# Kernel optimization log

Measured on AMD Instinct MI355X. Metric: run time of the kernel, lower is better.

The kernel has to match this reference:

```python
import jax, jax.numpy as jnp
import numpy as np

VOCAB, EMB, HID = 32000, 512, 512
B, S = 4, 2048


def _log_g(x):
    # log of g(x) where g(x) = x + 0.5 for x >= 0 else sigmoid(x)
    return jnp.where(x >= 0, jnp.log(jax.nn.relu(x) + 0.5), -jax.nn.softplus(-x))


def _layernorm(x, gamma, beta, eps):
    mu = jnp.mean(x, axis=-1, keepdims=True)
    var = jnp.mean(jnp.square(x - mu), axis=-1, keepdims=True)
    return (x - mu) * jax.lax.rsqrt(var + eps) * gamma + beta


def _mingru_layer(x, W):
    # x: [B,S,D_in], W: [D_in, 2*H] (no bias for minGRU)
    k, h_pre = jnp.split(x @ W, 2, axis=-1)          # gate pre-act, candidate pre-act
    log_coeffs = -jax.nn.softplus(k)                 # log(1 - z)
    log_b = -jax.nn.softplus(-k) + _log_g(h_pre)     # log(z) + log(g(h~))
    # Heinsen log-domain parallel scan along time axis
    a_star = jnp.cumsum(log_coeffs, axis=1)          # [B,S,H]
    log_h = a_star + jax.lax.cumlogsumexp(log_b - a_star, axis=1)
    return jnp.exp(log_h)


def setup_inputs() -> dict:
    key = jax.random.key(0)
    ks = jax.random.split(key, 8)
    s = 0.02
    return {
        "ids": jax.random.randint(ks[0], (B, S), 0, VOCAB, dtype=jnp.int32),
        "emb": jax.random.normal(ks[1], (VOCAB, EMB), jnp.float32) * s,
        "W0": jax.random.normal(ks[2], (EMB, 2 * HID), jnp.float32) * s,
        "W1": jax.random.normal(ks[3], (HID, 2 * HID), jnp.float32) * s,
        "ln0_g": jnp.ones((EMB,), jnp.float32),
        "ln0_b": jnp.zeros((EMB,), jnp.float32),
        "ln1_g": jnp.ones((HID,), jnp.float32),
        "ln1_b": jnp.zeros((HID,), jnp.float32),
        "lnf_g": jnp.ones((HID,), jnp.float32),
        "lnf_b": jnp.zeros((HID,), jnp.float32),
        "fc_w": jax.random.normal(ks[4], (HID, VOCAB), jnp.float32) * s,
        "fc_b": jnp.zeros((VOCAB,), jnp.float32),
    }


def reference(ids, emb, W0, W1, ln0_g, ln0_b, ln1_g, ln1_b, lnf_g, lnf_b, fc_w, fc_b):
    x = emb[ids]  # [B,S,EMB]
    for W, g, b in ((W0, ln0_g, ln0_b), (W1, ln1_g, ln1_b)):
        inp = x
        xn = _layernorm(x, g, b, 1e-5)           # pre-layer norm (cfg['norm']=True)
        x = _mingru_layer(xn, W) + inp           # residual=True, dropout=0
    x = _layernorm(x, lnf_g, lnf_b, 0.0)         # torch code passes bias as eps -> eps=0.0
    logits = x @ fc_w + fc_b                     # [B,S,VOCAB]
    return logits
```

## Files before the change

### kernel.cpp

```cpp
#include <hip/hip_runtime.h>

typedef __attribute__((ext_vector_type(8))) short short8;
typedef __attribute__((ext_vector_type(4))) float f32x4;
typedef __attribute__((ext_vector_type(8))) unsigned short u16x8;

#define B_ 4
#define S_ 2048
#define EMB_ 512
#define HID_ 512
#define VOCAB_ 32000
#define ROWS (B_ * S_)
#define NCHUNK 32
#define CHUNK 64

__device__ __forceinline__ unsigned short f2bf(float f) {
    unsigned int u = __float_as_uint(f);
    u += 0x7fffu + ((u >> 16) & 1u);
    return (unsigned short)(u >> 16);
}

__device__ __forceinline__ void gl_lds16(const unsigned short* g, unsigned short* l) {
    __builtin_amdgcn_global_load_lds(
        (const __attribute__((address_space(1))) unsigned int*)(uintptr_t)(g),
        (__attribute__((address_space(3))) unsigned int*)(unsigned int)(uintptr_t)(l),
        16, 0, 0);
}

__global__ __launch_bounds__(256) void transpose_convert_k(
    const float* __restrict__ src, unsigned short* __restrict__ dst, int K, int N) {
    __shared__ float t[32][33];
    int kt = blockIdx.y * 32, nt = blockIdx.x * 32;
    int tx = threadIdx.x & 31, ty = threadIdx.x >> 5;
#pragma unroll
    for (int i = 0; i < 4; i++)
        t[ty + i * 8][tx] = src[(size_t)(kt + ty + i * 8) * N + nt + tx];
    __syncthreads();
#pragma unroll
    for (int i = 0; i < 4; i++)
        dst[(size_t)(nt + ty + i * 8) * K + kt + tx] = f2bf(t[tx][ty + i * 8]);
}

__global__ __launch_bounds__(256) void prep_k(
    const int* __restrict__ ids, const float* __restrict__ emb,
    const float* __restrict__ gam, const float* __restrict__ bet,
    float* __restrict__ xres, unsigned short* __restrict__ xw,
    const float* __restrict__ W0, unsigned short* __restrict__ wt0,
    const float* __restrict__ W1, unsigned short* __restrict__ wt1,
    const float* __restrict__ fcw, unsigned short* __restrict__ fcwt) {
    __shared__ float t[32][33];
    int vb = blockIdx.x;
    int tid = threadIdx.x;
    if (vb < 2048) {
        int row = vb * 4 + (tid >> 6);
        int lane = tid & 63;
        const float4* src = (const float4*)(emb + (size_t)ids[row] * EMB_);
        float v[8];
        *(float4*)(v) = src[lane * 2];
        *(float4*)(v + 4) = src[lane * 2 + 1];
        float s = 0.f, s2 = 0.f;
#pragma unroll
        for (int j = 0; j < 8; j++) { s += v[j]; s2 += v[j] * v[j]; }
#pragma unroll
        for (int off = 1; off < 64; off <<= 1) {
            s += __shfl_xor(s, off);
            s2 += __shfl_xor(s2, off);
        }
        float mu = s * (1.f / EMB_);
        float var = fmaxf(s2 * (1.f / EMB_) - mu * mu, 0.f);
        float rstd = rsqrtf(var + 1e-5f);
        float4* xr = (float4*)(xres + (size_t)row * EMB_);
        xr[lane * 2] = *(float4*)(v);
        xr[lane * 2 + 1] = *(float4*)(v + 4);
        u16x8 o;
#pragma unroll
        for (int j = 0; j < 8; j++) {
            int c = lane * 8 + j;
            o[j] = f2bf((v[j] - mu) * rstd * gam[c] + bet[c]);
        }
        *(u16x8*)(xw + (size_t)row * EMB_ + lane * 8) = o;
        return;
    }
    vb -= 2048;
    const float* src;
    unsigned short* dst;
    int N;
    if (vb < 512)        { src = W0;  dst = wt0;  N = 1024; }
    else if (vb < 1024)  { vb -= 512;  src = W1;  dst = wt1;  N = 1024; }
    else                 { vb -= 1024; src = fcw; dst = fcwt; N = VOCAB_; }
    int ntiles = N >> 5;
    int ktile = vb / ntiles, ntile = vb - ktile * ntiles;
    int kt = ktile << 5, nt = ntile << 5;
    int tx = tid & 31, ty = tid >> 5;
#pragma unroll
    for (int i = 0; i < 4; i++)
        t[ty + i * 8][tx] = src[(size_t)(kt + ty + i * 8) * N + nt + tx];
    __syncthreads();
#pragma unroll
    for (int i = 0; i < 4; i++)
        dst[(size_t)(nt + ty + i * 8) * 512 + kt + tx] = f2bf(t[tx][ty + i * 8]);
}

__global__ __launch_bounds__(256) void ln_k(
    const float* __restrict__ xsrc,
    const float* __restrict__ gam, const float* __restrict__ bet,
    unsigned short* __restrict__ xw, float eps) {
    int row = blockIdx.x * 4 + (threadIdx.x >> 6);
    int lane = threadIdx.x & 63;
    const float4* src = (const float4*)(xsrc + (size_t)row * HID_);
    float v[8];
    *(float4*)(v) = src[lane * 2];
    *(float4*)(v + 4) = src[lane * 2 + 1];
    float s = 0.f, s2 = 0.f;
#pragma unroll
    for (int j = 0; j < 8; j++) { s += v[j]; s2 += v[j] * v[j]; }
#pragma unroll
    for (int off = 1; off < 64; off <<= 1) {
        s += __shfl_xor(s, off);
        s2 += __shfl_xor(s2, off);
    }
    float mu = s * (1.f / HID_);
    float var = fmaxf(s2 * (1.f / HID_) - mu * mu, 0.f);
    float rstd = rsqrtf(var + eps);
    u16x8 o;
#pragma unroll
    for (int j = 0; j < 8; j++) {
        int c = lane * 8 + j;
        o[j] = f2bf((v[j] - mu) * rstd * gam[c] + bet[c]);
    }
    *(u16x8*)(xw + (size_t)row * HID_ + lane * 8) = o;
}

__global__ __launch_bounds__(256) void gemm_bf16_k(
    const unsigned short* __restrict__ A, const unsigned short* __restrict__ Bt,
    float* __restrict__ C, int M, int N, int K) {
    __shared__ unsigned short lA[128 * 64];
    __shared__ unsigned short lB[128 * 64];
    __shared__ float eT[4][16 * 68];
    int tid = threadIdx.x;
    int w = tid >> 6, l = tid & 63;
    int m0 = blockIdx.y * 128, n0 = blockIdx.x * 128;
    int wm = w >> 1, wn = w & 1;
    f32x4 acc[4][4] = {};

    int rIn = l >> 3;
    int cOff = (l & 7) * 8;

    for (int k0 = 0; k0 < K; k0 += 64) {
#pragma unroll
        for (int i = 0; i < 4; i++) {
            int c = w * 4 + i;
            gl_lds16(A + (size_t)(m0 + c * 8 + rIn) * K + k0 + cOff, &lA[c * 512]);
            gl_lds16(Bt + (size_t)(n0 + c * 8 + rIn) * K + k0 + cOff, &lB[c * 512]);
        }
        asm volatile("s_waitcnt vmcnt(0)" ::: "memory");
        __syncthreads();

        const unsigned short* pa = lA + ((size_t)(wm * 64 + (l & 15)) * 64) + ((l >> 4) * 8);
        const unsigned short* pb = lB + ((size_t)(wn * 64 + (l & 15)) * 64) + ((l >> 4) * 8);
#pragma unroll
        for (int kk = 0; kk < 2; kk++) {
            short8 af[4], bfr[4];
#pragma unroll
            for (int m = 0; m < 4; m++) af[m] = *(const short8*)(pa + m * 16 * 64 + kk * 32);
#pragma unroll
            for (int n = 0; n < 4; n++) bfr[n] = *(const short8*)(pb + n * 16 * 64 + kk * 32);
#pragma unroll
            for (int m = 0; m < 4; m++)
#pragma unroll
                for (int n = 0; n < 4; n++)
                    acc[m][n] = __builtin_amdgcn_mfma_f32_16x16x32_bf16(af[m], bfr[n], acc[m][n], 0, 0, 0);
        }
        __syncthreads();
    }

    float* ep = eT[w];
    int rl = l >> 4, slot = l & 15;
    int rbase = m0 + wm * 64, cbase = n0 + wn * 64;
#pragma unroll
    for (int mf = 0; mf < 4; ++mf) {
#pragma unroll
        for (int nf = 0; nf < 4; ++nf)
#pragma unroll
            for (int j = 0; j < 4; ++j)
                ep[(rl * 4 + j) * 68 + nf * 16 + slot] = acc[mf][nf][j];
        asm volatile("s_waitcnt lgkmcnt(0)" ::: "memory");
#pragma unroll
        for (int p = 0; p < 4; ++p) {
            int r = p * 4 + rl;
            f32x4 vv = *(const f32x4*)(ep + r * 68 + slot * 4);
            *(f32x4*)(C + (size_t)(rbase + mf * 16 + r) * N + cbase + slot * 4) = vv;
        }
        asm volatile("s_waitcnt lgkmcnt(0)" ::: "memory");
    }
}

__device__ __forceinline__ void stage_half(
    const unsigned short* __restrict__ A, const unsigned short* __restrict__ Bt,
    int K, int m0, int n0, int nt, int H,
    char* smem, int r0, int c0, unsigned wq) {
    if (H >= 4 * nt) return;
    int T = H >> 2, j = H & 3;
    const unsigned short* src = (j < 2) ? A : Bt;
    int row0 = ((j < 2) ? m0 : n0) + ((j & 1) << 7);
    int k0 = T << 6;
    unsigned tb = ((unsigned)(T & 1) << 16) | ((unsigned)(j >> 1) << 15) | ((unsigned)(j & 1) << 14);
    const unsigned short* g0 = src + (size_t)(row0 + r0) * K + (k0 + c0);
    gl_lds16(g0, (unsigned short*)(smem + tb + wq));
    gl_lds16(g0 + (size_t)64 * K, (unsigned short*)(smem + tb + 8192 + wq));
}

#define MIDBAR() __builtin_amdgcn_s_barrier()
#define ENDBAR() do { asm volatile("s_waitcnt lgkmcnt(0)" ::: "memory"); \
                      asm volatile("s_barrier" ::: "memory"); } while (0)

#define PHASE_MFMA(AF, BF, MO, NO)                                                  \
    do {                                                                            \
        __builtin_amdgcn_s_setprio(1);                                             \
        _Pragma("unroll") for (int mf = 0; mf < 4; ++mf)                            \
        _Pragma("unroll") for (int nf = 0; nf < 2; ++nf)                            \
        _Pragma("unroll") for (int ks = 0; ks < 2; ++ks)                            \
            acc[(MO) + mf][(NO) + nf] = __builtin_amdgcn_mfma_f32_16x16x32_bf16(    \
                AF[mf][ks], BF[nf][ks], acc[(MO) + mf][(NO) + nf], 0, 0, 0);        \
        __builtin_amdgcn_s_setprio(0);                                             \
    } while (0)

__global__ __launch_bounds__(512, 2) void gemm256_bf16_k(
    const unsigned short* __restrict__ A, const unsigned short* __restrict__ Bt,
    const float* __restrict__ bias, float* __restrict__ C,
    int M, int N, int K, int nbn) {
    extern __shared__ char smem[];
    int tid = threadIdx.x;
    int w = tid >> 6, l = tid & 63;
    int wm = w >> 2, wn = w & 3;

    int nwg = gridDim.x;
    int bid = blockIdx.x;
    int swz = ((nwg & 7) == 0) ? ((bid & 7) * (nwg >> 3) + (bid >> 3)) : bid;
    int bm = swz / nbn, bn = swz % nbn;
    int m0 = bm << 8, n0 = bn << 8;

    int r0 = ((w >> 1) << 4) + (l >> 2);
    int c0 = ((w & 1) << 5) + (((l & 3) << 3) ^ ((l & 32) ? 16 : 0));
    unsigned wq = (unsigned)(w << 10);

    unsigned rowpart = (unsigned)(((l & 15) << 6) + (((((l >> 4) << 3)) ^ ((l & 8) ? 16 : 0)) << 1));
    unsigned aoff = ((unsigned)wm << 14) + rowpart;
    unsigned boff = 32768u + ((unsigned)wn << 13) + rowpart;

    int nt = K >> 6;
    f32x4 acc[8][4] = {};

    stage_half(A, Bt, K, m0, n0, nt, 0, smem, r0, c0, wq); asm volatile("" ::: "memory");
    stage_half(A, Bt, K, m0, n0, nt, 1, smem, r0, c0, wq); asm volatile("" ::: "memory");
    stage_half(A, Bt, K, m0, n0, nt, 2, smem, r0, c0, wq); asm volatile("" ::: "memory");
    stage_half(A, Bt, K, m0, n0, nt, 3, smem, r0, c0, wq); asm volatile("" ::: "memory");
    stage_half(A, Bt, K, m0, n0, nt, 4, smem, r0, c0, wq); asm volatile("" ::: "memory");
    stage_half(A, Bt, K, m0, n0, nt, 5, smem, r0, c0, wq);
    asm volatile("s_waitcnt vmcnt(4)" ::: "memory");
    asm volatile("s_barrier" ::: "memory");

    for (int t = 0; t < nt; ++t) {
        const char* pA = smem + (((unsigned)(t & 1)) << 16) + aoff;
        const char* pB = smem + (((unsigned)(t & 1)) << 16) + boff;
        short8 A0[4][2], A1[4][2], B0[2][2], B1[2][2];

#pragma unroll
        for (int mf = 0; mf < 4; ++mf)
#pragma unroll
            for (int ks = 0; ks < 2; ++ks)
                A0[mf][ks] = *(const short8*)(pA + mf * 2048 + ks * 1024);
#pragma unroll
        for (int nf = 0; nf < 2; ++nf)
#pragma unroll
            for (int ks = 0; ks < 2; ++ks)
                B0[nf][ks] = *(const short8*)(pB + nf * 2048 + ks * 1024);
        stage_half(A, Bt, K, m0, n0, nt, 4 * t + 6, smem, r0, c0, wq);
        MIDBAR();
        PHASE_MFMA(A0, B0, 0, 0);
        ENDBAR();

#pragma unroll
        for (int mf = 0; mf < 4; ++mf)
#pragma unroll
            for (int ks = 0; ks < 2; ++ks)
                A1[mf][ks] = *(const short8*)(pA + (4 + mf) * 2048 + ks * 1024);
#pragma unroll
        for (int nf = 0; nf < 2; ++nf)
#pragma unroll
            for (int ks = 0; ks < 2; ++ks)
                B1[nf][ks] = *(const short8*)(pB + (2 + nf) * 2048 + ks * 1024);
        stage_half(A, Bt, K, m0, n0, nt, 4 * t + 7, smem, r0, c0, wq);
        MIDBAR();
        PHASE_MFMA(A1, B0, 4, 0);
        ENDBAR();

        stage_half(A, Bt, K, m0, n0, nt, 4 * t + 8, smem, r0, c0, wq);
        MIDBAR();
        PHASE_MFMA(A1, B1, 4, 2);
        ENDBAR();

        stage_half(A, Bt, K, m0, n0, nt, 4 * t + 9, smem, r0, c0, wq);
        if (t < nt - 2)       { asm volatile("s_waitcnt vmcnt(4)" ::: "memory"); }
        else if (t == nt - 2) { asm volatile("s_waitcnt vmcnt(0)" ::: "memory"); }
        MIDBAR();
        PHASE_MFMA(A0, B1, 0, 2);
        ENDBAR();
    }

    float* ep = (float*)smem + w * (16 * 68);
    int rl = l >> 4, slot = l & 15;
    int rbase = m0 + (wm << 7), cbase = n0 + (wn << 6);
    float bs[4];
#pragma unroll
    for (int nf = 0; nf < 4; ++nf) bs[nf] = bias[cbase + nf * 16 + slot];
#pragma unroll
    for (int mf = 0; mf < 8; ++mf) {
#pragma unroll
        for (int nf = 0; nf < 4; ++nf)
#pragma unroll
            for (int j = 0; j < 4; ++j)
                ep[(rl * 4 + j) * 68 + nf * 16 + slot] = acc[mf][nf][j] + bs[nf];
        asm volatile("s_waitcnt lgkmcnt(0)" ::: "memory");
#pragma unroll
        for (int p = 0; p < 4; ++p) {
            int r = p * 4 + rl;
            f32x4 vv = *(const f32x4*)(ep + r * 68 + slot * 4);
            *(f32x4*)(C + (size_t)(rbase + mf * 16 + r) * N + cbase + slot * 4) = vv;
        }
        asm volatile("s_waitcnt lgkmcnt(0)" ::: "memory");
    }
}

__device__ __forceinline__ void gate_terms(float k, float hp, float& a, float& b) {
    float z = 1.f / (1.f + __expf(-k));
    a = 1.f - z;
    float g = (hp >= 0.f) ? (hp + 0.5f) : (1.f / (1.f + __expf(-hp)));
    b = z * g;
}

__global__ __launch_bounds__(256) void scan1_k(
    const float* __restrict__ proj, float* __restrict__ Ach, float* __restrict__ Bch) {
    int t = blockIdx.x * 256 + threadIdx.x;
    int h = t & (HID_ - 1);
    int bc = t >> 9;
    int b = bc >> 5, c = bc & (NCHUNK - 1);
    const float* p = proj + ((size_t)(b * S_ + c * CHUNK)) * (2 * HID_) + h;
    float A = 1.f, H = 0.f;
#pragma unroll 4
    for (int s = 0; s < CHUNK; s++) {
        float k = p[(size_t)s * (2 * HID_)];
        float hp = p[(size_t)s * (2 * HID_) + HID_];
        float a, bb;
        gate_terms(k, hp, a, bb);
        H = a * H + bb;
        A *= a;
    }
    Ach[t] = A;
    Bch[t] = H;
}

__global__ __launch_bounds__(256) void scan23_k(
    const float* __restrict__ proj, const float* __restrict__ Ach,
    const float* __restrict__ Bch, float* __restrict__ xres) {
    int t = blockIdx.x * 256 + threadIdx.x;
    int h = t & (HID_ - 1);
    int bc = t >> 9;
    int b = bc >> 5, c = bc & (NCHUNK - 1);
    float H = 0.f;
    for (int cp = 0; cp < c; cp++) {
        int idx = (b * NCHUNK + cp) * HID_ + h;
        H = Ach[idx] * H + Bch[idx];
    }
    const float* p = proj + ((size_t)(b * S_ + c * CHUNK)) * (2 * HID_) + h;
    float* x = xres + ((size_t)(b * S_ + c * CHUNK)) * HID_ + h;
#pragma unroll 4
    for (int s = 0; s < CHUNK; s++) {
        float k = p[(size_t)s * (2 * HID_)];
        float hp = p[(size_t)s * (2 * HID_) + HID_];
        float a, bb;
        gate_terms(k, hp, a, bb);
        H = a * H + bb;
        x[(size_t)s * HID_] += H;
    }
}

extern "C" void kernel_launch(void* const* d_in, const int* in_sizes, int n_in,
                              void* d_out, int out_size, void* d_ws, size_t ws_size,
                              hipStream_t stream) {
    const int* ids = (const int*)d_in[0];
    const float* emb = (const float*)d_in[1];
    const float* W0 = (const float*)d_in[2];
    const float* W1 = (const float*)d_in[3];
    const float* ln0_g = (const float*)d_in[4];
    const float* ln0_b = (const float*)d_in[5];
    const float* ln1_g = (const float*)d_in[6];
    const float* ln1_b = (const float*)d_in[7];
    const float* lnf_g = (const float*)d_in[8];
    const float* lnf_b = (const float*)d_in[9];
    const float* fc_w = (const float*)d_in[10];
    const float* fc_b = (const float*)d_in[11];
    float* out = (float*)d_out;

    (void)hipFuncSetAttribute((const void*)gemm256_bf16_k,
                              hipFuncAttributeMaxDynamicSharedMemorySize, 131072);

    char* ws = (char*)d_ws;
    const size_t OFF_XW   = 0;
    const size_t OFF_PROJ = 8388608;
    const size_t OFF_XRES = OFF_PROJ + 33554432;
    const size_t OFF_WT0  = OFF_XRES + 16777216;
    const size_t OFF_WT1  = OFF_WT0 + 1048576;
    const size_t OFF_SA   = OFF_WT1 + 1048576;
    const size_t OFF_SB   = OFF_SA + 262144;
    const size_t OFF_FCWT = OFF_SB + 262144;
    const size_t NEED_BIG = OFF_FCWT + 32768000;

    unsigned short* xw  = (unsigned short*)(ws + OFF_XW);
    float* proj         = (float*)(ws + OFF_PROJ);
    float* xres         = (float*)(ws + OFF_XRES);
    unsigned short* wt0 = (unsigned short*)(ws + OFF_WT0);
    unsigned short* wt1 = (unsigned short*)(ws + OFF_WT1);
    float* sA = (float*)(ws + OFF_SA);
    float* sB = (float*)(ws + OFF_SB);

    bool big = ws_size >= NEED_BIG;
    unsigned short* fcwt = big ? (unsigned short*)(ws + OFF_FCWT)
                               : (unsigned short*)(ws + OFF_PROJ);

    if (big) {
        prep_k<<<2048 + 1024 + 16000, 256, 0, stream>>>(
            ids, emb, ln0_g, ln0_b, xres, xw, W0, wt0, W1, wt1, fc_w, fcwt);
    } else {
        prep_k<<<2048 + 1024, 256, 0, stream>>>(
            ids, emb, ln0_g, ln0_b, xres, xw, W0, wt0, W1, wt1, fc_w, wt0);
    }

    gemm_bf16_k<<<dim3(1024 / 128, ROWS / 128), 256, 0, stream>>>(xw, wt0, proj, ROWS, 1024, 512);
    scan1_k<<<65536 / 256, 256, 0, stream>>>(proj, sA, sB);
    scan23_k<<<65536 / 256, 256, 0, stream>>>(proj, sA, sB, xres);

    ln_k<<<ROWS / 4, 256, 0, stream>>>(xres, ln1_g, ln1_b, xw, 1e-5f);
    gemm_bf16_k<<<dim3(1024 / 128, ROWS / 128), 256, 0, stream>>>(xw, wt1, proj, ROWS, 1024, 512);
    scan1_k<<<65536 / 256, 256, 0, stream>>>(proj, sA, sB);
    scan23_k<<<65536 / 256, 256, 0, stream>>>(proj, sA, sB, xres);

    ln_k<<<ROWS / 4, 256, 0, stream>>>(xres, lnf_g, lnf_b, xw, 0.0f);
    if (!big) {
        transpose_convert_k<<<dim3(VOCAB_ / 32, 512 / 32), 256, 0, stream>>>(fc_w, fcwt, 512, VOCAB_);
    }
    {
        int nbm = ROWS / 256, nbn = VOCAB_ / 256;
        gemm256_bf16_k<<<nbm * nbn, 512, 131072, stream>>>(xw, fcwt, fc_b, out, ROWS, VOCAB_, 512, nbn);
    }
}
```

Measured before the change: 580.0 us.

## Replace 256x256 vocab GEMM with 256x128 tile, K=32 steps, higher occupancy

The final logits GEMM now uses 256x128 output tiles with a K-step of 32 and a 48KB double-buffered LDS layout in place of 256x256 tiles with 128KB LDS. Launch bounds allow four workgroups per CU and the grid grows to 8000 blocks, with a fixed swizzle and an XOR-swizzled LDS layout. The aim is to fix the tile-count quantization on 32000 columns (125 column tiles of 256) and to raise occupancy so latency is hidden better. In exchange each tile reuses less data, there are more barriers per unit of MFMA work, and all shapes are hardcoded.

```diff
diff --git a/kernel.cpp b/kernel.cpp
--- a/kernel.cpp
+++ b/kernel.cpp
@@ -12,6 +12,8 @@
 #define ROWS (B_ * S_)
 #define NCHUNK 32
 #define CHUNK 64
+#define FK_ 512
+#define NT_F 16
 
 __device__ __forceinline__ unsigned short f2bf(float f) {
     unsigned int u = __float_as_uint(f);
@@ -194,127 +196,89 @@
     }
 }
 
-__device__ __forceinline__ void stage_half(
+__device__ __forceinline__ void stage3(
     const unsigned short* __restrict__ A, const unsigned short* __restrict__ Bt,
-    int K, int m0, int n0, int nt, int H,
-    char* smem, int r0, int c0, unsigned wq) {
-    if (H >= 4 * nt) return;
-    int T = H >> 2, j = H & 3;
-    const unsigned short* src = (j < 2) ? A : Bt;
-    int row0 = ((j < 2) ? m0 : n0) + ((j & 1) << 7);
-    int k0 = T << 6;
-    unsigned tb = ((unsigned)(T & 1) << 16) | ((unsigned)(j >> 1) << 15) | ((unsigned)(j & 1) << 14);
-    const unsigned short* g0 = src + (size_t)(row0 + r0) * K + (k0 + c0);
-    gl_lds16(g0, (unsigned short*)(smem + tb + wq));
-    gl_lds16(g0 + (size_t)64 * K, (unsigned short*)(smem + tb + 8192 + wq));
-}
-
-#define MIDBAR() __builtin_amdgcn_s_barrier()
-#define ENDBAR() do { asm volatile("s_waitcnt lgkmcnt(0)" ::: "memory"); \
-                      asm volatile("s_barrier" ::: "memory"); } while (0)
-
-#define PHASE_MFMA(AF, BF, MO, NO)                                                  \
-    do {                                                                            \
-        __builtin_amdgcn_s_setprio(1);                                             \
-        _Pragma("unroll") for (int mf = 0; mf < 4; ++mf)                            \
-        _Pragma("unroll") for (int nf = 0; nf < 2; ++nf)                            \
-        _Pragma("unroll") for (int ks = 0; ks < 2; ++ks)                            \
-            acc[(MO) + mf][(NO) + nf] = __builtin_amdgcn_mfma_f32_16x16x32_bf16(    \
-                AF[mf][ks], BF[nf][ks], acc[(MO) + mf][(NO) + nf], 0, 0, 0);        \
-        __builtin_amdgcn_s_setprio(0);                                             \
-    } while (0)
-
-__global__ __launch_bounds__(512, 2) void gemm256_bf16_k(
+    int bm, int bn, int T, char* smem, int rthr, int coff) {
+    if (T >= NT_F) return;
+    char* base = smem + (T & 1) * 24576;
+    int tid = threadIdx.x;
+    const unsigned short* ga = A + (size_t)(bm * 256 + rthr) * FK_ + T * 32 + coff;
+    gl_lds16(ga, (unsigned short*)(base + tid * 16));
+    gl_lds16(ga + (size_t)128 * FK_, (unsigned short*)(base + 8192 + tid * 16));
+    const unsigned short* gb = Bt + (size_t)(bn * 128 + rthr) * FK_ + T * 32 + coff;
+    gl_lds16(gb, (unsigned short*)(base + 16384 + tid * 16));
+}
+
+__global__ __launch_bounds__(512, 4) void gemmF2_k(
     const unsigned short* __restrict__ A, const unsigned short* __restrict__ Bt,
-    const float* __restrict__ bias, float* __restrict__ C,
-    int M, int N, int K, int nbn) {
+    const float* __restrict__ bias, float* __restrict__ C) {
     extern __shared__ char smem[];
     int tid = threadIdx.x;
     int w = tid >> 6, l = tid & 63;
-    int wm = w >> 2, wn = w & 3;
-
-    int nwg = gridDim.x;
+    int wm = w >> 1, wn = w & 1;
+
     int bid = blockIdx.x;
-    int swz = ((nwg & 7) == 0) ? ((bid & 7) * (nwg >> 3) + (bid >> 3)) : bid;
-    int bm = swz / nbn, bn = swz % nbn;
-    int m0 = bm << 8, n0 = bn << 8;
-
-    int r0 = ((w >> 1) << 4) + (l >> 2);
-    int c0 = ((w & 1) << 5) + (((l & 3) << 3) ^ ((l & 32) ? 16 : 0));
-    unsigned wq = (unsigned)(w << 10);
-
-    unsigned rowpart = (unsigned)(((l & 15) << 6) + (((((l >> 4) << 3)) ^ ((l & 8) ? 16 : 0)) << 1));
-    unsigned aoff = ((unsigned)wm << 14) + rowpart;
-    unsigned boff = 32768u + ((unsigned)wn << 13) + rowpart;
-
-    int nt = K >> 6;
-    f32x4 acc[8][4] = {};
-
-    stage_half(A, Bt, K, m0, n0, nt, 0, smem, r0, c0, wq); asm volatile("" ::: "memory");
-    stage_half(A, Bt, K, m0, n0, nt, 1, smem, r0, c0, wq); asm volatile("" ::: "memory");
-    stage_half(A, Bt, K, m0, n0, nt, 2, smem, r0, c0, wq); asm volatile("" ::: "memory");
-    stage_half(A, Bt, K, m0, n0, nt, 3, smem, r0, c0, wq); asm volatile("" ::: "memory");
-    stage_half(A, Bt, K, m0, n0, nt, 4, smem, r0, c0, wq); asm volatile("" ::: "memory");
-    stage_half(A, Bt, K, m0, n0, nt, 5, smem, r0, c0, wq);
-    asm volatile("s_waitcnt vmcnt(4)" ::: "memory");
+    int swz = (bid & 7) * 1000 + (bid >> 3);
+    int bn = swz / 32, bm = swz % 32;
+
+    int rthr = tid >> 2;
+    int swt = ((tid >> 2) ^ (tid >> 4)) & 3;
+    int coff = ((tid & 3) ^ swt) << 3;
+
+    int swl = ((l & 3) ^ ((l >> 2) & 3));
+    int slotb = (((l >> 4) ^ swl) << 4);
+    int aoffb = (wm * 64 + (l & 15)) * 64 + slotb;
+    int boffb = 16384 + (wn * 64 + (l & 15)) * 64 + slotb;
+
+    f32x4 acc[4][4] = {};
+
+    stage3(A, Bt, bm, bn, 0, smem, rthr, coff);
+    asm volatile("" ::: "memory");
+    stage3(A, Bt, bm, bn, 1, smem, rthr, coff);
+    asm volatile("s_waitcnt vmcnt(3)" ::: "memory");
     asm volatile("s_barrier" ::: "memory");
 
-    for (int t = 0; t < nt; ++t) {
-        const char* pA = smem + (((unsigned)(t & 1)) << 16) + aoff;
-        const char* pB = smem + (((unsigned)(t & 1)) << 16) + boff;
-        short8 A0[4][2], A1[4][2], B0[2][2], B1[2][2];
-
-#pragma unroll
-        for (int mf = 0; mf < 4; ++mf)
-#pragma unroll
-            for (int ks = 0; ks < 2; ++ks)
-                A0[mf][ks] = *(const short8*)(pA + mf * 2048 + ks * 1024);
-#pragma unroll
-        for (int nf = 0; nf < 2; ++nf)
-#pragma unroll
-            for (int ks = 0; ks < 2; ++ks)
-                B0[nf][ks] = *(const short8*)(pB + nf * 2048 + ks * 1024);
-        stage_half(A, Bt, K, m0, n0, nt, 4 * t + 6, smem, r0, c0, wq);
-        MIDBAR();
-        PHASE_MFMA(A0, B0, 0, 0);
-        ENDBAR();
-
-#pragma unroll
-        for (int mf = 0; mf < 4; ++mf)
-#pragma unroll
-            for (int ks = 0; ks < 2; ++ks)
-                A1[mf][ks] = *(const short8*)(pA + (4 + mf) * 2048 + ks * 1024);
-#pragma unroll
-        for (int nf = 0; nf < 2; ++nf)
-#pragma unroll
-            for (int ks = 0; ks < 2; ++ks)
-                B1[nf][ks] = *(const short8*)(pB + (2 + nf) * 2048 + ks * 1024);
-        stage_half(A, Bt, K, m0, n0, nt, 4 * t + 7, smem, r0, c0, wq);
-        MIDBAR();
-        PHASE_MFMA(A1, B0, 4, 0);
-        ENDBAR();
-
-        stage_half(A, Bt, K, m0, n0, nt, 4 * t + 8, smem, r0, c0, wq);
-        MIDBAR();
-        PHASE_MFMA(A1, B1, 4, 2);
-        ENDBAR();
-
-        stage_half(A, Bt, K, m0, n0, nt, 4 * t + 9, smem, r0, c0, wq);
-        if (t < nt - 2)       { asm volatile("s_waitcnt vmcnt(4)" ::: "memory"); }
-        else if (t == nt - 2) { asm volatile("s_waitcnt vmcnt(0)" ::: "memory"); }
-        MIDBAR();
-        PHASE_MFMA(A0, B1, 0, 2);
-        ENDBAR();
+    for (int t = 0; t < NT_F; ++t) {
+        const char* base = smem + (t & 1) * 24576;
+        short8 Af[4], Bf[4];
+#pragma unroll
+        for (int mf = 0; mf < 4; ++mf) Af[mf] = *(const short8*)(base + aoffb + mf * 1024);
+#pragma unroll
+        for (int nf = 0; nf < 4; ++nf) Bf[nf] = *(const short8*)(base + boffb + nf * 1024);
+        __builtin_amdgcn_s_barrier();
+        __builtin_amdgcn_s_setprio(1);
+#pragma unroll
+        for (int mf = 0; mf < 2; ++mf)
+#pragma unroll
+            for (int nf = 0; nf < 4; ++nf)
+                acc[mf][nf] = __builtin_amdgcn_mfma_f32_16x16x32_bf16(Af[mf], Bf[nf], acc[mf][nf], 0, 0, 0);
+        __builtin_amdgcn_s_setprio(0);
+        asm volatile("s_waitcnt lgkmcnt(0)" ::: "memory");
+        asm volatile("s_barrier" ::: "memory");
+
+        stage3(A, Bt, bm, bn, t + 2, smem, rthr, coff);
+        if (t < NT_F - 2)       { asm volatile("s_waitcnt vmcnt(3)" ::: "memory"); }
+        else if (t == NT_F - 2) { asm volatile("s_waitcnt vmcnt(0)" ::: "memory"); }
+        __builtin_amdgcn_s_barrier();
+        __builtin_amdgcn_s_setprio(1);
+#pragma unroll
+        for (int mf = 2; mf < 4; ++mf)
+#pragma unroll
+            for (int nf = 0; nf < 4; ++nf)
+                acc[mf][nf] = __builtin_amdgcn_mfma_f32_16x16x32_bf16(Af[mf], Bf[nf], acc[mf][nf], 0, 0, 0);
+        __builtin_amdgcn_s_setprio(0);
+        asm volatile("s_waitcnt lgkmcnt(0)" ::: "memory");
+        asm volatile("s_barrier" ::: "memory");
     }
 
     float* ep = (float*)smem + w * (16 * 68);
     int rl = l >> 4, slot = l & 15;
-    int rbase = m0 + (wm << 7), cbase = n0 + (wn << 6);
+    int rbase = bm * 256 + wm * 64, cbase = bn * 128 + wn * 64;
     float bs[4];
 #pragma unroll
     for (int nf = 0; nf < 4; ++nf) bs[nf] = bias[cbase + nf * 16 + slot];
 #pragma unroll
-    for (int mf = 0; mf < 8; ++mf) {
+    for (int mf = 0; mf < 4; ++mf) {
 #pragma unroll
         for (int nf = 0; nf < 4; ++nf)
 #pragma unroll
@@ -325,7 +289,7 @@
         for (int p = 0; p < 4; ++p) {
             int r = p * 4 + rl;
             f32x4 vv = *(const f32x4*)(ep + r * 68 + slot * 4);
-            *(f32x4*)(C + (size_t)(rbase + mf * 16 + r) * N + cbase + slot * 4) = vv;
+            *(f32x4*)(C + (size_t)(rbase + mf * 16 + r) * VOCAB_ + cbase + slot * 4) = vv;
         }
         asm volatile("s_waitcnt lgkmcnt(0)" ::: "memory");
     }
@@ -401,8 +365,8 @@
     const float* fc_b = (const float*)d_in[11];
     float* out = (float*)d_out;
 
-    (void)hipFuncSetAttribute((const void*)gemm256_bf16_k,
-                              hipFuncAttributeMaxDynamicSharedMemorySize, 131072);
+    (void)hipFuncSetAttribute((const void*)gemmF2_k,
+                              hipFuncAttributeMaxDynamicSharedMemorySize, 49152);
 
     char* ws = (char*)d_ws;
     const size_t OFF_XW   = 0;
@@ -448,8 +412,5 @@
     if (!big) {
         transpose_convert_k<<<dim3(VOCAB_ / 32, 512 / 32), 256, 0, stream>>>(fc_w, fcwt, 512, VOCAB_);
     }
-    {
-        int nbm = ROWS / 256, nbn = VOCAB_ / 256;
-        gemm256_bf16_k<<<nbm * nbn, 512, 131072, stream>>>(xw, fcwt, fc_b, out, ROWS, VOCAB_, 512, nbn);
-    }
-}
+    gemmF2_k<<<8000, 512, 49152, stream>>>(xw, fcwt, fc_b, out);
+}
```

Result: slower. 760.2 us (+31.1%).
